# Performance work log

Measured on AMD Instinct MI355X. Metric: run time of the kernel, lower is better.

Reference implementation:

```python
import jax, jax.numpy as jnp
import numpy as np

L, C, FC, H, W, K = 6, 256, 1024, 4, 10, 3
B, T = 4, 1024
KC = C // H


def _get_rel_emb(emb, length):
    # emb: [1, 2W+1, KC] -> [1, 2*length-1, KC]
    pad_len = max(length - (W + 1), 0)
    start = max(W + 1 - length, 0)
    if pad_len > 0:
        emb = jnp.pad(emb, ((0, 0), (pad_len, pad_len), (0, 0)))
    return emb[:, start:start + 2 * length - 1]


def _rel_to_abs(x):
    # [b,h,l,2l-1] -> [b,h,l,l] via pad/reshape shift trick
    b, h, l, _ = x.shape
    x = jnp.pad(x, ((0, 0), (0, 0), (0, 0), (0, 1)))
    x = x.reshape(b, h, l * 2 * l)
    x = jnp.pad(x, ((0, 0), (0, 0), (0, l - 1)))
    return x.reshape(b, h, l + 1, 2 * l - 1)[:, :, :l, l - 1:]


def _abs_to_rel(x):
    # [b,h,l,l] -> [b,h,l,2l-1]
    b, h, l, _ = x.shape
    x = jnp.pad(x, ((0, 0), (0, 0), (0, 0), (0, l - 1)))
    x = x.reshape(b, h, l * l + l * (l - 1))
    x = jnp.pad(x, ((0, 0), (0, 0), (l, 0)))
    return x.reshape(b, h, l, 2 * l)[:, :, :, 1:]


def _ln(x, g, b, eps=1e-5):
    # channel-wise LayerNorm over dim 1 of [B,C,T]
    m = x.mean(axis=1, keepdims=True)
    v = ((x - m) ** 2).mean(axis=1, keepdims=True)
    return (x - m) * jax.lax.rsqrt(v + eps) * g[None, :, None] + b[None, :, None]


def _conv1(x, w, b):
    # pointwise Conv1d: x [B,Cin,T], w [Cout,Cin]
    return jnp.einsum('oc,bct->bot', w, x) + b[None, :, None]


def _convk(x, w, b):
    # Conv1d: x [B,Cin,Tpad], w [Cout,Cin,K], VALID
    y = jax.lax.conv_general_dilated(x, w, (1,), 'VALID', dimension_numbers=('NCH', 'OIH', 'NCH'))
    return y + b[None, :, None]


def _attn(x, mask, wq, bq, wk, bk, wv, bv, wo, bo, erk, erv):
    b, d, t = x.shape
    q = _conv1(x, wq, bq)
    k = _conv1(x, wk, bk)
    v = _conv1(x, wv, bv)
    def split(z):
        return z.reshape(b, H, KC, t).transpose(0, 1, 3, 2)  # [b,h,t,kc]
    qh = split(q) / np.sqrt(KC).astype(np.float32)
    kh = split(k)
    vh = split(v)
    scores = jnp.einsum('bhld,bhmd->bhlm', qh, kh)
    rel_k = _get_rel_emb(erk, t)[0]  # [2t-1, kc]
    scores = scores + _rel_to_abs(jnp.einsum('bhld,md->bhlm', qh, rel_k))
    scores = jnp.where(mask == 0, jnp.float32(-1e4), scores)
    p = jax.nn.softmax(scores, axis=-1)
    out = jnp.einsum('bhlm,bhmd->bhld', p, vh)
    rel_v = _get_rel_emb(erv, t)[0]
    out = out + jnp.einsum('bhlm,md->bhld', _abs_to_rel(p), rel_v)
    out = out.transpose(0, 1, 3, 2).reshape(b, d, t)
    return _conv1(out, wo, bo)


def _ffn(x, mask, w1, b1, w2, b2):
    pl, pr = (K - 1) // 2, K // 2
    def pad_t(z):
        return jnp.pad(z * mask, ((0, 0), (0, 0), (pl, pr)))
    h = jax.nn.relu(_convk(pad_t(x), w1, b1))
    return _convk(pad_t(h), w2, b2) * mask


def setup_inputs() -> dict:
    key = jax.random.key(0)
    ks = jax.random.split(key, 12)
    s = 0.05
    return {
        'x': jax.random.normal(ks[0], (B, C, T), jnp.float32),
        'x_mask': jnp.ones((B, 1, T), jnp.float32),
        'wq': s * jax.random.normal(ks[1], (L, C, C), jnp.float32),
        'bq': jnp.zeros((L, C), jnp.float32),
        'wk': s * jax.random.normal(ks[2], (L, C, C), jnp.float32),
        'bk': jnp.zeros((L, C), jnp.float32),
        'wv': s * jax.random.normal(ks[3], (L, C, C), jnp.float32),
        'bv': jnp.zeros((L, C), jnp.float32),
        'wo': s * jax.random.normal(ks[4], (L, C, C), jnp.float32),
        'bo': jnp.zeros((L, C), jnp.float32),
        'erk': (KC ** -0.5) * jax.random.normal(ks[5], (L, 1, 2 * W + 1, KC), jnp.float32),
        'erv': (KC ** -0.5) * jax.random.normal(ks[6], (L, 1, 2 * W + 1, KC), jnp.float32),
        'ln1_g': jnp.ones((L, C), jnp.float32),
        'ln1_b': jnp.zeros((L, C), jnp.float32),
        'ffn_w1': s * jax.random.normal(ks[7], (L, FC, C, K), jnp.float32),
        'ffn_b1': jnp.zeros((L, FC), jnp.float32),
        'ffn_w2': s * jax.random.normal(ks[8], (L, C, FC, K), jnp.float32),
        'ffn_b2': jnp.zeros((L, C), jnp.float32),
        'ln2_g': jnp.ones((L, C), jnp.float32),
        'ln2_b': jnp.zeros((L, C), jnp.float32),
    }


def reference(x, x_mask, wq, bq, wk, bk, wv, bv, wo, bo, erk, erv, ln1_g, ln1_b, ffn_w1, ffn_b1, ffn_w2, ffn_b2, ln2_g, ln2_b):
    attn_mask = x_mask[:, :, None, :] * x_mask[:, :, :, None]  # [B,1,T,T]
    x = x * x_mask
    for i in range(L):
        y = _attn(x, attn_mask, wq[i], bq[i], wk[i], bk[i], wv[i], bv[i], wo[i], bo[i], erk[i], erv[i])
        x = _ln(x + y, ln1_g[i], ln1_b[i])
        y = _ffn(x, x_mask, ffn_w1[i], ffn_b1[i], ffn_w2[i], ffn_b2[i])
        x = _ln(x + y, ln2_g[i], ln2_b[i])
    return x * x_mask
```

## Files before the change

kernel.cpp:

```cpp
#include <hip/hip_runtime.h>


#define Lz 6
#define Cz 256
#define FCz 1024
#define Hz 4
#define Wz 10
#define Bz 4
#define Tz 1024
#define KCz 64
#define NR 21
#define TS 1032
#define PADF 4
#define PROWS 1026
#define MFIX 8.0f

typedef unsigned short u16;
typedef unsigned int u32;
typedef __attribute__((ext_vector_type(8))) short bf8v;
typedef __attribute__((ext_vector_type(4))) float f4v;

#define MFMA(a, b, c) __builtin_amdgcn_mfma_f32_16x16x32_bf16(a, b, c, 0, 0, 0)

__device__ inline void bf_split(float v, u16& hi, u16& lo) {
  unsigned u = __float_as_uint(v);
  unsigned hr = (u + 0x7FFFu + ((u >> 16) & 1u)) >> 16;
  float rem = v - __uint_as_float(hr << 16);
  unsigned u2 = __float_as_uint(rem);
  unsigned lr = (u2 + 0x7FFFu + ((u2 >> 16) & 1u)) >> 16;
  hi = (u16)hr;
  lo = (u16)lr;
}

__device__ inline u16 bf_rne(float v) {
  u32 u = __float_as_uint(v);
  return (u16)((u + 0x7FFFu + ((u >> 16) & 1u)) >> 16);
}

__global__ __launch_bounds__(256) void mask_in(const float* __restrict__ x,
                                               const float* __restrict__ m,
                                               float* __restrict__ xp) {
  int id = blockIdx.x * 256 + threadIdx.x;
  if (id < Bz * Cz * Tz) {
    int t = id & (Tz - 1), row = id >> 10, b = id >> 18;
    xp[(size_t)row * TS + PADF + t] = x[id] * m[b * Tz + t];
  }
}

__global__ __launch_bounds__(256) void mask_out(const float* __restrict__ xp,
                                                const float* __restrict__ m,
                                                float* __restrict__ out) {
  int id = blockIdx.x * 256 + threadIdx.x;
  if (id < Bz * Cz * Tz) {
    int t = id & (Tz - 1), row = id >> 10, b = id >> 18;
    out[id] = xp[(size_t)row * TS + PADF + t] * m[b * Tz + t];
  }
}

__global__ __launch_bounds__(256) void zero_halo(u16* hi, u16* lo, int Cd) {
  int id = blockIdx.x * 256 + threadIdx.x;
  if (id >= Bz * 2 * Cd) return;
  int c = id % Cd, rb = id / Cd, b = rb >> 1, s = rb & 1;
  size_t a = ((size_t)b * PROWS + (s ? (PROWS - 1) : 0)) * Cd + c;
  hi[a] = 0;
  lo[a] = 0;
}

__global__ __launch_bounds__(256) void tpack(const float* __restrict__ src,
                                             const float* __restrict__ mask,
                                             u16* __restrict__ dhi,
                                             u16* __restrict__ dlo, int Cd) {
  __shared__ float L[64 * 68];
  const int tid = threadIdx.x;
  const int t0 = blockIdx.x * 64, c0 = blockIdx.y * 64, b = blockIdx.z;
  const float* sb = src + (size_t)b * Cd * TS + PADF;
#pragma unroll
  for (int i = 0; i < 16; i++) {
    int id = tid + 256 * i;
    int cc = id >> 6, tt = id & 63;
    L[cc * 68 + tt] = sb[(size_t)(c0 + cc) * TS + t0 + tt];
  }
  __syncthreads();
  const int tt = tid >> 2, p = tid & 3;
  float mv = mask[(size_t)b * Tz + t0 + tt];
  u16 hs[16], ls[16];
#pragma unroll
  for (int j = 0; j < 16; j++) {
    float v = L[(p * 16 + j) * 68 + tt] * mv;
    bf_split(v, hs[j], ls[j]);
  }
  size_t da = ((size_t)b * PROWS + t0 + tt + 1) * Cd + c0 + p * 16;
  *(uint4*)&dhi[da] = *(uint4*)&hs[0];
  *(uint4*)&dhi[da + 8] = *(uint4*)&hs[8];
  *(uint4*)&dlo[da] = *(uint4*)&ls[0];
  *(uint4*)&dlo[da + 8] = *(uint4*)&ls[8];
}

__global__ __launch_bounds__(256) void pack_all(
    const float* __restrict__ wq, const float* __restrict__ wk,
    const float* __restrict__ wv, const float* __restrict__ wo_,
    const float* __restrict__ bq, const float* __restrict__ bk,
    const float* __restrict__ bv, const float* __restrict__ bo,
    const float* __restrict__ erk, const float* __restrict__ erv,
    const float* __restrict__ fw1, const float* __restrict__ fw2,
    u16* __restrict__ qwAll, float* __restrict__ pbAll,
    u16* __restrict__ ekAll, u16* __restrict__ evAll,
    u16* __restrict__ w1All, u16* __restrict__ w2All) {
  const int blk = blockIdx.x, tid = threadIdx.x;
  const int layer = blk / 7184;
  const int bl = blk % 7184;
  if (bl < 1024) {
    int id = bl * 256 + tid;
    int o = id >> 8, c = id & 255;
    int sel = o >> 8;
    const size_t wof = (size_t)layer * Cz * Cz;
    const float* w = sel == 0 ? wq + wof
                              : (sel == 1 ? wk + wof
                                          : (sel == 2 ? wv + wof : wo_ + wof));
    qwAll[(size_t)layer * 262144 + id] = bf_rne(w[((o & 255) << 8) + c]);
    if (id < 1024) {
      int s2 = id >> 8;
      const float* bs = s2 == 0 ? bq : (s2 == 1 ? bk : (s2 == 2 ? bv : bo));
      pbAll[layer * 1024 + id] = bs[layer * Cz + (id & 255)];
    }
  } else if (bl < 1040) {
    int id = (bl - 1024) * 256 + tid;
    if (id < 2048) {
      int rr = id >> 6, d = id & 63;
      ekAll[layer * 2048 + id] =
          bf_rne((rr < NR) ? erk[(size_t)layer * NR * KCz + rr * KCz + d]
                           : 0.f);
    } else {
      int id2 = id - 2048;
      int d = id2 >> 5, rr = id2 & 31;
      evAll[layer * 2048 + id2] =
          bf_rne((rr < NR) ? erv[(size_t)layer * NR * KCz + rr * KCz + d]
                           : 0.f);
    }
  } else if (bl < 4112) {
    int id = (bl - 1040) * 256 + tid;
    int c = id % Cz;
    int rest = id / Cz;
    int o = rest % FCz, tap = rest / FCz;
    w1All[(size_t)layer * 786432 + id] =
        bf_rne(fw1[(size_t)layer * FCz * Cz * 3 + ((size_t)o * Cz + c) * 3 +
                   tap]);
  } else {
    int id = (bl - 4112) * 256 + tid;
    int c = id % FCz;
    int rest = id / FCz;
    int o = rest % Cz, tap = rest / Cz;
    w2All[(size_t)layer * 786432 + id] =
        bf_rne(fw2[(size_t)layer * Cz * FCz * 3 + ((size_t)o * FCz + c) * 3 +
                   tap]);
  }
}

template <int EPI>
__global__ __launch_bounds__(256) void mfma_gemm2(
    const u16* __restrict__ Ah, const u16* __restrict__ Bh,
    const u16* __restrict__ Bl, const float* __restrict__ bias,
    const float* __restrict__ mask, float* __restrict__ out,
    float* __restrict__ out2, u16* __restrict__ pqh, u16* __restrict__ pql,
    u16* __restrict__ pkh, u16* __restrict__ pvh, int M, int Kc, int m_base) {
  __shared__ __align__(16) char smraw[17408];
  u16* Ash = (u16*)smraw;
  u16* Bsh = Ash + 2560;
  u16* Bsl = Bsh + 2560;
  const int tid = threadIdx.x;
  const int lane = tid & 63, wid = tid >> 6;
  const int wm = wid & 1, wn = wid >> 1;
  const int r = lane & 15, qd = lane >> 4;
  const int t0 = blockIdx.x * 64;
  const int b = blockIdx.z;
  const int srow = tid >> 2, sseg = (tid & 3) * 8;

  int m0, kc0, kcN;
  float* outp = out;
  if constexpr (EPI == 3) {
    m0 = m_base + (blockIdx.y >> 1) * 64;
    kc0 = (blockIdx.y & 1) * (Kc / 2);
    kcN = Kc / 2;
    outp = (blockIdx.y & 1) ? out2 : out;
  } else {
    m0 = blockIdx.y * 64 + m_base;
    kc0 = 0;
    kcN = Kc;
  }

  f4v acc[2][2];
#pragma unroll
  for (int i = 0; i < 2; i++)
#pragma unroll
    for (int j = 0; j < 2; j++) acc[i][j] = (f4v)(0.f);

  const size_t arow = (size_t)(m0 + srow) * Kc + kc0;
  const size_t brow = ((size_t)b * PROWS + t0 + 1 + srow) * Kc + kc0;
  for (int kc = 0; kc < kcN; kc += 32) {
    *(uint4*)&Ash[srow * 40 + sseg] = *(const uint4*)&Ah[arow + kc + sseg];
    *(uint4*)&Bsh[srow * 40 + sseg] = *(const uint4*)&Bh[brow + kc + sseg];
    *(uint4*)&Bsl[srow * 40 + sseg] = *(const uint4*)&Bl[brow + kc + sseg];
    __syncthreads();
    bf8v ah[2], bh2[2], bl2[2];
#pragma unroll
    for (int f = 0; f < 2; f++) {
      int ar = (wm * 32 + f * 16 + r) * 40 + qd * 8;
      int br = (wn * 32 + f * 16 + r) * 40 + qd * 8;
      ah[f] = *(bf8v*)&Ash[ar];
      bh2[f] = *(bf8v*)&Bsh[br];
      bl2[f] = *(bf8v*)&Bsl[br];
    }
#pragma unroll
    for (int mf = 0; mf < 2; mf++)
#pragma unroll
      for (int nf = 0; nf < 2; nf++) {
        acc[mf][nf] = MFMA(ah[mf], bh2[nf], acc[mf][nf]);
        acc[mf][nf] = MFMA(ah[mf], bl2[nf], acc[mf][nf]);
      }
    __syncthreads();
  }

  float* Ds = (float*)smraw;
  if constexpr (EPI == 0) {
    const int sel = m0 >> 8;
    const int h = (m0 >> 6) & 3;
    const int bhI = b * Hz + h;
    if (sel < 2) {
#pragma unroll
      for (int mf = 0; mf < 2; mf++)
#pragma unroll
        for (int nf = 0; nf < 2; nf++) {
          int nl = wn * 32 + nf * 16 + r;
          int ml = wm * 32 + mf * 16 + qd * 4;
          *(f4v*)&Ds[nl * 68 + ml] = acc[mf][nf];
        }
      __syncthreads();
      const int row = tid >> 2, p = tid & 3;
      size_t da = ((size_t)bhI * Tz + t0 + row) * KCz + p * 16;
      if (sel == 0) {
        u16 hs[16], ls[16];
#pragma unroll
        for (int jj = 0; jj < 4; jj++) {
          float4 dv = *(float4*)&Ds[row * 68 + p * 16 + jj * 4];
          float4 bb = *(const float4*)&bias[m0 + p * 16 + jj * 4];
          float vv[4] = {(dv.x + bb.x) * 0.125f, (dv.y + bb.y) * 0.125f,
                         (dv.z + bb.z) * 0.125f, (dv.w + bb.w) * 0.125f};
#pragma unroll
          for (int e = 0; e < 4; e++)
            bf_split(vv[e], hs[jj * 4 + e], ls[jj * 4 + e]);
        }
        *(uint4*)&pqh[da] = *(uint4*)&hs[0];
        *(uint4*)&pqh[da + 8] = *(uint4*)&hs[8];
        *(uint4*)&pql[da] = *(uint4*)&ls[0];
        *(uint4*)&pql[da + 8] = *(uint4*)&ls[8];
      } else {
        u16 hs[16];
#pragma unroll
        for (int jj = 0; jj < 4; jj++) {
          float4 dv = *(float4*)&Ds[row * 68 + p * 16 + jj * 4];
          float4 bb = *(const float4*)&bias[m0 + p * 16 + jj * 4];
          hs[jj * 4 + 0] = bf_rne(dv.x + bb.x);
          hs[jj * 4 + 1] = bf_rne(dv.y + bb.y);
          hs[jj * 4 + 2] = bf_rne(dv.z + bb.z);
          hs[jj * 4 + 3] = bf_rne(dv.w + bb.w);
        }
        *(uint4*)&pkh[da] = *(uint4*)&hs[0];
        *(uint4*)&pkh[da + 8] = *(uint4*)&hs[8];
      }
    } else {
#pragma unroll
      for (int mf = 0; mf < 2; mf++)
#pragma unroll
        for (int nf = 0; nf < 2; nf++) {
          int ml = wm * 32 + mf * 16 + qd * 4;
          int nl = wn * 32 + nf * 16 + r;
#pragma unroll
          for (int e = 0; e < 4; e++) Ds[(ml + e) * 68 + nl] = acc[mf][nf][e];
        }
      __syncthreads();
      const int row = tid >> 2, p = tid & 3;
      const float bb = bias[m0 + row];
      u16 hs[16];
#pragma unroll
      for (int jj = 0; jj < 16; jj++)
        hs[jj] = bf_rne(Ds[row * 68 + p * 16 + jj] + bb);
      size_t da = ((size_t)bhI * KCz + row) * Tz + t0 + p * 16;
      *(uint4*)&pvh[da] = *(uint4*)&hs[0];
      *(uint4*)&pvh[da + 8] = *(uint4*)&hs[8];
    }
  } else {
#pragma unroll
    for (int mf = 0; mf < 2; mf++)
#pragma unroll
      for (int nf = 0; nf < 2; nf++) {
        int ml = wm * 32 + mf * 16 + qd * 4;
        int nl = wn * 32 + nf * 16 + r;
#pragma unroll
        for (int e = 0; e < 4; e++) Ds[(ml + e) * 68 + nl] = acc[mf][nf][e];
      }
    __syncthreads();
    const int row = tid >> 2, p = tid & 3;
    size_t oa = ((size_t)b * Cz + (m0 - m_base) + row) * Tz + t0 + p * 16;
#pragma unroll
    for (int jj = 0; jj < 4; jj++)
      *(float4*)&outp[oa + jj * 4] = *(float4*)&Ds[row * 68 + p * 16 + jj * 4];
  }
}

template <int EPI>
__global__ __launch_bounds__(256, 2) void conv_mfma(
    const u16* __restrict__ Ah, const u16* __restrict__ Bh,
    const u16* __restrict__ Bl, const float* __restrict__ bias,
    const float* __restrict__ mask, u16* __restrict__ ph,
    u16* __restrict__ pl, float* __restrict__ o0, float* __restrict__ o1,
    float* __restrict__ o2, float* __restrict__ o3, int M, int Kc) {
  __shared__ __align__(16) char smraw[36480];
  u16* Ash = (u16*)smraw;
  u16* Bsh = Ash + 3 * 64 * 40;
  u16* Bsl = Bsh + 132 * 40;
  const int tid = threadIdx.x;
  const int lane = tid & 63, wn = tid >> 6;
  const int r = lane & 15, qd = lane >> 4;
  const int t0 = blockIdx.x * 128;
  const int b = blockIdx.z;

  int m0, kc0, kcN;
  float* outp = nullptr;
  if constexpr (EPI == 3) {
    int mt = blockIdx.y >> 2, sp = blockIdx.y & 3;
    m0 = mt * 64;
    kc0 = sp * (Kc / 4);
    kcN = Kc / 4;
    outp = sp == 0 ? o0 : (sp == 1 ? o1 : (sp == 2 ? o2 : o3));
  } else {
    m0 = blockIdx.y * 64;
    kc0 = 0;
    kcN = Kc;
  }

  const int srow = tid >> 2, sseg = (tid & 3) * 8;
  const bool btail = tid < 8;
  const int brow2 = 128 + (tid >> 2);

  f4v acc[4][2];
#pragma unroll
  for (int i = 0; i < 4; i++)
#pragma unroll
    for (int j = 0; j < 2; j++) acc[i][j] = (f4v)(0.f);

  const size_t abase = (size_t)(m0 + srow) * Kc + kc0 + sseg;
  const size_t bbase = ((size_t)b * PROWS + t0 + srow) * Kc + kc0 + sseg;
  const size_t bbase64 = bbase + (size_t)64 * Kc;
  const size_t bbaseT = ((size_t)b * PROWS + t0 + brow2) * Kc + kc0 + sseg;

  uint4 ar[3], bh0, bh1, bl0, bl1, bht, blt;
  auto LOADR = [&](int kc) {
#pragma unroll
    for (int tp = 0; tp < 3; tp++)
      ar[tp] = *(const uint4*)&Ah[(size_t)tp * M * Kc + abase + kc];
    bh0 = *(const uint4*)&Bh[bbase + kc];
    bh1 = *(const uint4*)&Bh[bbase64 + kc];
    bl0 = *(const uint4*)&Bl[bbase + kc];
    bl1 = *(const uint4*)&Bl[bbase64 + kc];
    if (btail) {
      bht = *(const uint4*)&Bh[bbaseT + kc];
      blt = *(const uint4*)&Bl[bbaseT + kc];
    }
  };

  LOADR(0);
  for (int kc = 0; kc < kcN; kc += 32) {
#pragma unroll
    for (int tp = 0; tp < 3; tp++)
      *(uint4*)&Ash[(tp * 64 + srow) * 40 + sseg] = ar[tp];
    *(uint4*)&Bsh[srow * 40 + sseg] = bh0;
    *(uint4*)&Bsh[(srow + 64) * 40 + sseg] = bh1;
    *(uint4*)&Bsl[srow * 40 + sseg] = bl0;
    *(uint4*)&Bsl[(srow + 64) * 40 + sseg] = bl1;
    if (btail) {
      *(uint4*)&Bsh[brow2 * 40 + sseg] = bht;
      *(uint4*)&Bsl[brow2 * 40 + sseg] = blt;
    }
    __syncthreads();
    if (kc + 32 < kcN) LOADR(kc + 32);
#pragma unroll
    for (int tap = 0; tap < 3; tap++) {
      bf8v ah[4], bh2[2], bl2[2];
#pragma unroll
      for (int mf = 0; mf < 4; mf++)
        ah[mf] = *(bf8v*)&Ash[(tap * 64 + mf * 16 + r) * 40 + qd * 8];
#pragma unroll
      for (int nf = 0; nf < 2; nf++) {
        int br = (wn * 32 + nf * 16 + r + tap) * 40 + qd * 8;
        bh2[nf] = *(bf8v*)&Bsh[br];
        bl2[nf] = *(bf8v*)&Bsl[br];
      }
#pragma unroll
      for (int mf = 0; mf < 4; mf++)
#pragma unroll
        for (int nf = 0; nf < 2; nf++) {
          acc[mf][nf] = MFMA(ah[mf], bh2[nf], acc[mf][nf]);
          acc[mf][nf] = MFMA(ah[mf], bl2[nf], acc[mf][nf]);
        }
    }
    __syncthreads();
  }

  if constexpr (EPI == 1) {
    float* Ds = (float*)smraw;
#pragma unroll
    for (int mf = 0; mf < 4; mf++)
#pragma unroll
      for (int nf = 0; nf < 2; nf++) {
        int tl = wn * 32 + nf * 16 + r;
        int ml = mf * 16 + qd * 4;
        *(f4v*)&Ds[tl * 68 + ml] = acc[mf][nf];
      }
    __syncthreads();
    const int row = tid >> 1, half = (tid & 1) * 32;
    const int t = t0 + row;
    const float mv = mask[(size_t)b * Tz + t];
    u16 hs[32], ls[32];
#pragma unroll
    for (int j = 0; j < 32; j += 4) {
      float4 dv = *(float4*)&Ds[row * 68 + half + j];
      float4 bb = *(const float4*)&bias[m0 + half + j];
      float vv[4] = {dv.x + bb.x, dv.y + bb.y, dv.z + bb.z, dv.w + bb.w};
#pragma unroll
      for (int e = 0; e < 4; e++) {
        float v = fmaxf(vv[e], 0.f) * mv;
        bf_split(v, hs[j + e], ls[j + e]);
      }
    }
    size_t da = ((size_t)b * PROWS + t + 1) * M + m0 + half;
#pragma unroll
    for (int j = 0; j < 32; j += 8) {
      *(uint4*)&ph[da + j] = *(uint4*)&hs[j];
      *(uint4*)&pl[da + j] = *(uint4*)&ls[j];
    }
  } else {
    float* Ds = (float*)smraw;
#pragma unroll
    for (int mf = 0; mf < 4; mf++)
#pragma unroll
      for (int nf = 0; nf < 2; nf++) {
        int ml = mf * 16 + qd * 4;
        int nl = wn * 32 + nf * 16 + r;
#pragma unroll
        for (int e = 0; e < 4; e++) Ds[(ml + e) * 132 + nl] = acc[mf][nf][e];
      }
    __syncthreads();
    const int row = tid >> 2, seg = (tid & 3) * 32;
    size_t oa = ((size_t)b * Cz + m0 + row) * Tz + t0 + seg;
#pragma unroll
    for (int j = 0; j < 8; j++)
      *(float4*)&outp[oa + j * 4] = *(float4*)&Ds[row * 132 + seg + j * 4];
  }
}

__global__ __launch_bounds__(128, 2) void attn_mfma(
    const u16* __restrict__ Qh_, const u16* __restrict__ Ql_,
    const u16* __restrict__ Kh_, const u16* __restrict__ Vh_,
    const float* __restrict__ mask, const u16* __restrict__ erkH,
    const u16* __restrict__ ervH, float* __restrict__ O0,
    float* __restrict__ O1, float* __restrict__ O2, float* __restrict__ O3,
    float* __restrict__ lp0, float* __restrict__ lp1,
    float* __restrict__ lp2, float* __restrict__ lp3) {
  __shared__ __align__(16) char smraw[2][14336];
  const int tid = threadIdx.x;
  const int lane = tid & 63, wid = tid >> 6;
  const int r = lane & 15, qd = lane >> 4;
  const int idx = blockIdx.x;
  const int bh = idx & 15;
  const int split = (idx >> 4) & 3;
  const int i0w = (idx >> 6) * 64 + wid * 32;
  const int b = bh >> 2, h = bh & 3;
  const float* mb = mask + (size_t)b * Tz;
  const size_t qkbase = (size_t)bh * Tz * KCz;
  const size_t vbase = (size_t)bh * KCz * Tz;
  float* Op = split == 0 ? O0 : (split == 1 ? O1 : (split == 2 ? O2 : O3));
  float* lp = split == 0 ? lp0 : (split == 1 ? lp1 : (split == 2 ? lp2 : lp3));
  const int j0beg = split * 256;

  float* rqs = (float*)(smraw[wid]);
  float* bands = rqs + 704;
  u16* Pp = (u16*)(smraw[wid] + 5632);

  bf8v qh[2][2], ql[2][2];
#pragma unroll
  for (int rs = 0; rs < 2; rs++) {
    const size_t qrow = qkbase + (size_t)(i0w + rs * 16 + r) * KCz;
#pragma unroll
    for (int ks = 0; ks < 2; ks++) {
      qh[rs][ks] = *(const bf8v*)&Qh_[qrow + ks * 32 + qd * 8];
      ql[rs][ks] = *(const bf8v*)&Ql_[qrow + ks * 32 + qd * 8];
    }
  }
  for (int t = lane; t < 704; t += 64) bands[t] = -1e30f;

#pragma unroll
  for (int rs = 0; rs < 2; rs++) {
    f4v rc[2] = {(f4v)(0.f), (f4v)(0.f)};
#pragma unroll
    for (int nf = 0; nf < 2; nf++)
#pragma unroll
      for (int ks = 0; ks < 2; ks++) {
        bf8v eh = *(const bf8v*)&erkH[(16 * nf + r) * 64 + ks * 32 + qd * 8];
        rc[nf] = MFMA(qh[rs][ks], eh, rc[nf]);
        rc[nf] = MFMA(ql[rs][ks], eh, rc[nf]);
      }
#pragma unroll
    for (int nf = 0; nf < 2; nf++) {
      int rr = 16 * nf + r;
      if (rr < NR) {
#pragma unroll
        for (int e = 0; e < 4; e++)
          rqs[(rs * 16 + 4 * qd + e) * 22 + rr] = rc[nf][e];
      }
    }
  }

  float qm[2][4];
#pragma unroll
  for (int rs = 0; rs < 2; rs++)
#pragma unroll
    for (int e = 0; e < 4; e++) qm[rs][e] = mb[i0w + rs * 16 + 4 * qd + e];

  float lacc[2][4] = {};
  f4v oacc[2][4];
#pragma unroll
  for (int rs = 0; rs < 2; rs++)
#pragma unroll
    for (int nf = 0; nf < 4; nf++) oacc[rs][nf] = (f4v)(0.f);

#pragma unroll 2
  for (int jt = 0; jt < 4; jt++) {
    const int j0 = j0beg + jt * 64;
    bf8v kh[4][2], vh[4][2];
#pragma unroll
    for (int nf = 0; nf < 4; nf++) {
      const size_t kr = qkbase + (size_t)(j0 + 16 * nf + r) * KCz;
      const size_t vr = vbase + (size_t)(16 * nf + r) * Tz + j0;
#pragma unroll
      for (int ks = 0; ks < 2; ks++) {
        kh[nf][ks] = *(const bf8v*)&Kh_[kr + ks * 32 + qd * 8];
        vh[nf][ks] = *(const bf8v*)&Vh_[vr + ks * 32 + qd * 8];
      }
    }
    float km4[4];
#pragma unroll
    for (int nf = 0; nf < 4; nf++) km4[nf] = mb[j0 + 16 * nf + r];

#pragma unroll
    for (int rs = 0; rs < 2; rs++) {
      f4v sa[4];
#pragma unroll
      for (int nf = 0; nf < 4; nf++) sa[nf] = (f4v)(0.f);
#pragma unroll
      for (int nf = 0; nf < 4; nf++)
#pragma unroll
        for (int ks = 0; ks < 2; ks++) {
          sa[nf] = MFMA(qh[rs][ks], kh[nf][ks], sa[nf]);
          sa[nf] = MFMA(ql[rs][ks], kh[nf][ks], sa[nf]);
        }
      const int ibase = i0w + rs * 16;
      const bool diag = (j0 + 63 >= ibase - Wz) && (j0 <= ibase + 15 + Wz);
#pragma unroll
      for (int nf = 0; nf < 4; nf++)
#pragma unroll
        for (int e = 0; e < 4; e++) {
          const int iloc = rs * 16 + 4 * qd + e;
          float s = sa[nf][e];
          if (diag) {
            int dl = (j0 + 16 * nf + r) - (i0w + iloc);
            bool inb = (unsigned)(dl + Wz) <= 2u * Wz;
            if (inb) s += rqs[iloc * 22 + dl + Wz];
            if (qm[rs][e] * km4[nf] == 0.f) s = -1e4f;
            if (inb) bands[iloc * 22 + dl + Wz] = s;
          } else {
            if (qm[rs][e] * km4[nf] == 0.f) s = -1e4f;
          }
          float p = __expf(s - MFIX);
          lacc[rs][e] += p;
          Pp[iloc * 72 + 16 * nf + r] = bf_rne(p);
        }
    }
#pragma unroll
    for (int rs = 0; rs < 2; rs++)
#pragma unroll
      for (int ks = 0; ks < 2; ks++) {
        bf8v Ph = *(bf8v*)&Pp[(rs * 16 + r) * 72 + ks * 32 + qd * 8];
#pragma unroll
        for (int nf = 0; nf < 4; nf++)
          oacc[rs][nf] = MFMA(Ph, vh[nf][ks], oacc[rs][nf]);
      }
  }

  for (int t = lane; t < 32 * 32; t += 64) {
    int i = t >> 5, rr = t & 31;
    float p = (rr < NR) ? __expf(bands[i * 22 + rr] - MFIX) : 0.f;
    Pp[i * 72 + rr] = bf_rne(p);
  }
#pragma unroll
  for (int rs = 0; rs < 2; rs++) {
    bf8v Ph = *(bf8v*)&Pp[(rs * 16 + r) * 72 + qd * 8];
#pragma unroll
    for (int nf = 0; nf < 4; nf++) {
      bf8v eh = *(const bf8v*)&ervH[(16 * nf + r) * 32 + qd * 8];
      oacc[rs][nf] = MFMA(Ph, eh, oacc[rs][nf]);
    }
  }

#pragma unroll
  for (int off = 1; off < 16; off <<= 1)
#pragma unroll
    for (int rs = 0; rs < 2; rs++)
#pragma unroll
      for (int e = 0; e < 4; e++)
        lacc[rs][e] += __shfl_xor(lacc[rs][e], off, 16);
  if (r == 0) {
#pragma unroll
    for (int rs = 0; rs < 2; rs++)
#pragma unroll
      for (int e = 0; e < 4; e++)
        lp[(size_t)bh * Tz + i0w + rs * 16 + 4 * qd + e] = lacc[rs][e];
  }

  float* Os = (float*)Pp;
#pragma unroll
  for (int rs = 0; rs < 2; rs++)
#pragma unroll
    for (int nf = 0; nf < 4; nf++)
#pragma unroll
      for (int e = 0; e < 4; e++)
        Os[(rs * 16 + 4 * qd + e) * 68 + 16 * nf + r] = oacc[rs][nf][e];
#pragma unroll
  for (int rs = 0; rs < 2; rs++) {
    const float* src = &Os[(rs * 16 + r) * 68 + qd * 16];
    size_t oa = ((size_t)bh * Tz + i0w + rs * 16 + r) * KCz + qd * 16;
#pragma unroll
    for (int jj = 0; jj < 4; jj++)
      *(float4*)&Op[oa + jj * 4] = *(const float4*)&src[jj * 4];
  }
}

__global__ __launch_bounds__(256) void attn_combine(
    const float* __restrict__ O0, const float* __restrict__ O1,
    const float* __restrict__ O2, const float* __restrict__ O3,
    const float* __restrict__ l0, const float* __restrict__ l1,
    const float* __restrict__ l2, const float* __restrict__ l3,
    u16* __restrict__ outH, u16* __restrict__ outL,
    u16* __restrict__ hpH, u16* __restrict__ hpL) {
  const int bh = blockIdx.y, b = bh >> 2, h = bh & 3;
  if (blockIdx.x == 0) {
    int id = bh * 256 + threadIdx.x;
#pragma unroll
    for (int kk = 0; kk < 2; kk++) {
      int k = id + kk * 4096;
      int c = k & (FCz - 1), rb = k >> 10, bb2 = rb >> 1, ss = rb & 1;
      size_t a = ((size_t)bb2 * PROWS + (ss ? (PROWS - 1) : 0)) * FCz + c;
      hpH[a] = 0;
      hpL[a] = 0;
    }
  }
  const int i = blockIdx.x * 16 + (threadIdx.x >> 4);
  const int d0 = (threadIdx.x & 15) * 4;
  const size_t oa = ((size_t)bh * Tz + i) * KCz + d0;
  float4 a = *(const float4*)&O0[oa];
  float4 c = *(const float4*)&O1[oa];
  float4 d = *(const float4*)&O2[oa];
  float4 f = *(const float4*)&O3[oa];
  const size_t la = (size_t)bh * Tz + i;
  const float li = 1.f / (l0[la] + l1[la] + l2[la] + l3[la]);
  float v[4] = {(a.x + c.x + d.x + f.x) * li, (a.y + c.y + d.y + f.y) * li,
                (a.z + c.z + d.z + f.z) * li, (a.w + c.w + d.w + f.w) * li};
  u16 hs[4], ls[4];
#pragma unroll
  for (int e = 0; e < 4; e++) bf_split(v[e], hs[e], ls[e]);
  size_t da = ((size_t)b * PROWS + i + 1) * Cz + h * 64 + d0;
  *(uint2*)&outH[da] = *(uint2*)&hs[0];
  *(uint2*)&outL[da] = *(uint2*)&ls[0];
}

template <int VAR, int NP>
__global__ __launch_bounds__(256) void fused_ln(
    float* __restrict__ x, const float* __restrict__ y,
    const float* __restrict__ p1, const float* __restrict__ p2,
    const float* __restrict__ p3, const float* __restrict__ cbias,
    const float* __restrict__ g, const float* __restrict__ bb,
    const float* __restrict__ mask, u16* __restrict__ dhi,
    u16* __restrict__ dlo) {
  __shared__ float L[256 * 9];
  __shared__ float red[32][8], red2[32][8];
  __shared__ float ms[8], rs[8];
  const int tid = threadIdx.x;
  const int t0 = blockIdx.x * 8, b = blockIdx.y;
  const int tl = tid & 7, grp = tid >> 3;
  const size_t bx = (size_t)b * Cz * TS + PADF + t0 + tl;
  const size_t by = (size_t)b * Cz * Tz + t0 + tl;
  const float mv = mask[(size_t)b * Tz + t0 + tl];
  float s = 0.f, sq = 0.f;
#pragma unroll
  for (int i = 0; i < 8; i++) {
    int c = grp + i * 32;
    float add = y[by + (size_t)c * Tz] + p1[by + (size_t)c * Tz] + cbias[c];
    if constexpr (NP == 4)
      add += p2[by + (size_t)c * Tz] + p3[by + (size_t)c * Tz];
    if constexpr (VAR == 1) add *= mv;
    float v = x[bx + (size_t)c * TS] + add;
    L[c * 9 + tl] = v;
    s += v;
    sq += v * v;
  }
  red[grp][tl] = s;
  red2[grp][tl] = sq;
  __syncthreads();
  if (tid < 64) {
    const int j = tid >> 3, tt = tid & 7;
    float su = red[j][tt] + red[j + 8][tt] + red[j + 16][tt] + red[j + 24][tt];
    float sqq =
        red2[j][tt] + red2[j + 8][tt] + red2[j + 16][tt] + red2[j + 24][tt];
    su += __shfl_xor(su, 8);
    su += __shfl_xor(su, 16);
    su += __shfl_xor(su, 32);
    sqq += __shfl_xor(sqq, 8);
    sqq += __shfl_xor(sqq, 16);
    sqq += __shfl_xor(sqq, 32);
    if (j == 0) {
      float m = su * (1.f / Cz);
      ms[tt] = m;
      rs[tt] = rsqrtf(sqq * (1.f / Cz) - m * m + 1e-5f);
    }
  }
  __syncthreads();
  const float m = ms[tl], r = rs[tl];
#pragma unroll
  for (int i = 0; i < 8; i++) {
    int c = grp + i * 32;
    float v = (L[c * 9 + tl] - m) * r * g[c] + bb[c];
    x[bx + (size_t)c * TS] = v;
    L[c * 9 + tl] = v * mv;
  }
  __syncthreads();
  const int tt = tid & 7, p = tid >> 3;
  u16 hs[8], ls[8];
#pragma unroll
  for (int j = 0; j < 8; j++)
    bf_split(L[(p * 8 + j) * 9 + tt], hs[j], ls[j]);
  size_t da = ((size_t)b * PROWS + t0 + tt + 1) * Cz + p * 8;
  *(uint4*)&dhi[da] = *(uint4*)&hs[0];
  *(uint4*)&dlo[da] = *(uint4*)&ls[0];
}

extern "C" void kernel_launch(void* const* d_in, const int* in_sizes, int n_in,
                              void* d_out, int out_size, void* d_ws,
                              size_t ws_size, hipStream_t stream) {
  const float* x = (const float*)d_in[0];
  const float* xm = (const float*)d_in[1];
  const float* wq = (const float*)d_in[2];
  const float* bq = (const float*)d_in[3];
  const float* wk = (const float*)d_in[4];
  const float* bk = (const float*)d_in[5];
  const float* wv = (const float*)d_in[6];
  const float* bv = (const float*)d_in[7];
  const float* wo = (const float*)d_in[8];
  const float* bo = (const float*)d_in[9];
  const float* erk = (const float*)d_in[10];
  const float* erv = (const float*)d_in[11];
  const float* g1 = (const float*)d_in[12];
  const float* b1 = (const float*)d_in[13];
  const float* fw1 = (const float*)d_in[14];
  const float* fb1 = (const float*)d_in[15];
  const float* fw2 = (const float*)d_in[16];
  const float* fb2 = (const float*)d_in[17];
  const float* g2 = (const float*)d_in[18];
  const float* b2 = (const float*)d_in[19];

  const size_t NBC = (size_t)Bz * Cz * Tz;
  const size_t XBN = (size_t)Bz * Cz * TS;
  const size_t HP = (size_t)Bz * PROWS * FCz;
  const size_t XP = (size_t)Bz * PROWS * Cz;
  const size_t QS = (size_t)Bz * Hz * Tz * KCz;

  float* ws = (float*)d_ws;
  float* xb = ws;
  float* yb = xb + XBN;
  float* p1 = yb + NBC;
  float* p2 = p1 + NBC;
  float* p3 = p2 + NBC;
  float* unf = p3 + NBC;
  u16* hpH = (u16*)unf;
  u16* hpL = hpH + HP;
  u16* Qh = (u16*)unf;
  u16* Ql = Qh + QS;
  u16* Kh = Ql + QS;
  u16* Vh = Kh + QS;
  float* xpf = unf + HP;
  u16* xpH = (u16*)xpf;
  u16* xpL = xpH + XP;
  float* qwf = xpf + XP;
  u16* qwAll = (u16*)qwf;
  float* w1f = qwf + 786432;
  u16* w1All = (u16*)w1f;
  float* w2f = w1f + 2359296;
  u16* w2All = (u16*)w2f;
  float* erf = w2f + 2359296;
  u16* ekAll = (u16*)erf;
  u16* evAll = ekAll + 12288;
  float* pbAll = erf + 12288;
  float* lb0 = pbAll + 6144;
  float* lb1 = lb0 + 16384;
  float* lb2 = lb1 + 16384;
  float* lb3 = lb2 + 16384;

  const int ntot = (int)NBC;
  pack_all<<<dim3(6 * 7184), 256, 0, stream>>>(
      wq, wk, wv, wo, bq, bk, bv, bo, erk, erv, fw1, fw2, qwAll, pbAll, ekAll,
      evAll, w1All, w2All);
  mask_in<<<dim3((ntot + 255) / 256), 256, 0, stream>>>(x, xm, xb);
  zero_halo<<<dim3((Bz * 2 * Cz + 255) / 256), 256, 0, stream>>>(xpH, xpL, Cz);
  tpack<<<dim3(16, 4, 4), 256, 0, stream>>>(xb, xm, xpH, xpL, Cz);

  for (int l = 0; l < Lz; l++) {
    mfma_gemm2<0><<<dim3(16, 12, 4), 256, 0, stream>>>(
        qwAll + (size_t)l * 262144, xpH, xpL, pbAll + l * 1024, xm, nullptr,
        nullptr, Qh, Ql, Kh, Vh, 1024, Cz, 0);
    attn_mfma<<<dim3(1024), 128, 0, stream>>>(
        Qh, Ql, Kh, Vh, xm, ekAll + l * 2048, evAll + l * 2048, yb, p1, p2, p3,
        lb0, lb1, lb2, lb3);
    attn_combine<<<dim3(64, 16), 256, 0, stream>>>(yb, p1, p2, p3, lb0, lb1,
                                                   lb2, lb3, xpH, xpL, hpH,
                                                   hpL);
    mfma_gemm2<3><<<dim3(16, 8, 4), 256, 0, stream>>>(
        qwAll + (size_t)l * 262144, xpH, xpL, pbAll + l * 1024, xm, yb, p1,
        nullptr, nullptr, nullptr, nullptr, 1024, Cz, 768);
    fused_ln<2, 2><<<dim3(128, 4), 256, 0, stream>>>(
        xb, yb, p1, nullptr, nullptr, bo + l * Cz, g1 + l * Cz, b1 + l * Cz,
        xm, xpH, xpL);
    conv_mfma<1><<<dim3(8, 16, 4), 256, 0, stream>>>(
        w1All + (size_t)l * 786432, xpH, xpL, fb1 + l * FCz, xm, hpH, hpL,
        nullptr, nullptr, nullptr, nullptr, FCz, Cz);
    conv_mfma<3><<<dim3(8, 16, 4), 256, 0, stream>>>(
        w2All + (size_t)l * 786432, hpH, hpL, nullptr, xm, nullptr, nullptr,
        yb, p1, p2, p3, Cz, FCz);
    fused_ln<1, 4><<<dim3(128, 4), 256, 0, stream>>>(
        xb, yb, p1, p2, p3, fb2 + l * Cz, g2 + l * Cz, b2 + l * Cz, xm, xpH,
        xpL);
  }
  mask_out<<<dim3((ntot + 255) / 256), 256, 0, stream>>>(xb, xm,
                                                         (float*)d_out);
}
```

Before: 992.0 us.

## Fuse attention split-combine into output-projection GEMM and zero conv halos in-register

```diff
diff --git a/kernel.cpp b/kernel.cpp
--- a/kernel.cpp
+++ b/kernel.cpp
@@ -55,15 +55,6 @@
     int t = id & (Tz - 1), row = id >> 10, b = id >> 18;
     out[id] = xp[(size_t)row * TS + PADF + t] * m[b * Tz + t];
   }
-}
-
-__global__ __launch_bounds__(256) void zero_halo(u16* hi, u16* lo, int Cd) {
-  int id = blockIdx.x * 256 + threadIdx.x;
-  if (id >= Bz * 2 * Cd) return;
-  int c = id % Cd, rb = id / Cd, b = rb >> 1, s = rb & 1;
-  size_t a = ((size_t)b * PROWS + (s ? (PROWS - 1) : 0)) * Cd + c;
-  hi[a] = 0;
-  lo[a] = 0;
 }
 
 __global__ __launch_bounds__(256) void tpack(const float* __restrict__ src,
@@ -160,9 +151,13 @@
 __global__ __launch_bounds__(256) void mfma_gemm2(
     const u16* __restrict__ Ah, const u16* __restrict__ Bh,
     const u16* __restrict__ Bl, const float* __restrict__ bias,
-    const float* __restrict__ mask, float* __restrict__ out,
-    float* __restrict__ out2, u16* __restrict__ pqh, u16* __restrict__ pql,
-    u16* __restrict__ pkh, u16* __restrict__ pvh, int M, int Kc, int m_base) {
+    float* __restrict__ out, float* __restrict__ out2,
+    u16* __restrict__ pqh, u16* __restrict__ pql, u16* __restrict__ pkh,
+    u16* __restrict__ pvh, const float* __restrict__ Ox0,
+    const float* __restrict__ Ox1, const float* __restrict__ Ox2,
+    const float* __restrict__ Ox3, const float* __restrict__ sl0,
+    const float* __restrict__ sl1, const float* __restrict__ sl2,
+    const float* __restrict__ sl3, int M, int Kc, int m_base) {
   __shared__ __align__(16) char smraw[17408];
   u16* Ash = (u16*)smraw;
   u16* Bsh = Ash + 2560;
@@ -198,8 +193,37 @@
   const size_t brow = ((size_t)b * PROWS + t0 + 1 + srow) * Kc + kc0;
   for (int kc = 0; kc < kcN; kc += 32) {
     *(uint4*)&Ash[srow * 40 + sseg] = *(const uint4*)&Ah[arow + kc + sseg];
-    *(uint4*)&Bsh[srow * 40 + sseg] = *(const uint4*)&Bh[brow + kc + sseg];
-    *(uint4*)&Bsl[srow * 40 + sseg] = *(const uint4*)&Bl[brow + kc + sseg];
+    if constexpr (EPI == 3) {
+      const int cc = kc0 + kc + sseg;
+      const int hh = cc >> 6, dd = cc & 63;
+      const size_t lbi = (size_t)(b * Hz + hh) * Tz + t0 + srow;
+      const size_t ob = lbi * KCz + dd;
+      float4 qa = *(const float4*)&Ox0[ob];
+      float4 qb = *(const float4*)&Ox0[ob + 4];
+      float4 ra = *(const float4*)&Ox1[ob];
+      float4 rb = *(const float4*)&Ox1[ob + 4];
+      float4 sa = *(const float4*)&Ox2[ob];
+      float4 sb = *(const float4*)&Ox2[ob + 4];
+      float4 ta = *(const float4*)&Ox3[ob];
+      float4 tb = *(const float4*)&Ox3[ob + 4];
+      const float li = 1.f / (sl0[lbi] + sl1[lbi] + sl2[lbi] + sl3[lbi]);
+      float v[8] = {(qa.x + ra.x + sa.x + ta.x) * li,
+                    (qa.y + ra.y + sa.y + ta.y) * li,
+                    (qa.z + ra.z + sa.z + ta.z) * li,
+                    (qa.w + ra.w + sa.w + ta.w) * li,
+                    (qb.x + rb.x + sb.x + tb.x) * li,
+                    (qb.y + rb.y + sb.y + tb.y) * li,
+                    (qb.z + rb.z + sb.z + tb.z) * li,
+                    (qb.w + rb.w + sb.w + tb.w) * li};
+      u16 hhs[8], lls[8];
+#pragma unroll
+      for (int e = 0; e < 8; e++) bf_split(v[e], hhs[e], lls[e]);
+      *(uint4*)&Bsh[srow * 40 + sseg] = *(uint4*)&hhs[0];
+      *(uint4*)&Bsl[srow * 40 + sseg] = *(uint4*)&lls[0];
+    } else {
+      *(uint4*)&Bsh[srow * 40 + sseg] = *(const uint4*)&Bh[brow + kc + sseg];
+      *(uint4*)&Bsl[srow * 40 + sseg] = *(const uint4*)&Bl[brow + kc + sseg];
+    }
     __syncthreads();
     bf8v ah[2], bh2[2], bl2[2];
 #pragma unroll
@@ -341,6 +365,9 @@
   const int srow = tid >> 2, sseg = (tid & 3) * 8;
   const bool btail = tid < 8;
   const int brow2 = 128 + (tid >> 2);
+  const bool h0 = (t0 + srow == 0);
+  const bool hT = btail && (t0 + brow2 == PROWS - 1);
+  const uint4 z4 = {0u, 0u, 0u, 0u};
 
   f4v acc[4][2];
 #pragma unroll
@@ -359,12 +386,20 @@
     for (int tp = 0; tp < 3; tp++)
       ar[tp] = *(const uint4*)&Ah[(size_t)tp * M * Kc + abase + kc];
     bh0 = *(const uint4*)&Bh[bbase + kc];
+    bl0 = *(const uint4*)&Bl[bbase + kc];
+    if (h0) {
+      bh0 = z4;
+      bl0 = z4;
+    }
     bh1 = *(const uint4*)&Bh[bbase64 + kc];
-    bl0 = *(const uint4*)&Bl[bbase + kc];
     bl1 = *(const uint4*)&Bl[bbase64 + kc];
     if (btail) {
       bht = *(const uint4*)&Bh[bbaseT + kc];
       blt = *(const uint4*)&Bl[bbaseT + kc];
+      if (hT) {
+        bht = z4;
+        blt = z4;
+      }
     }
   };
 
@@ -644,44 +679,6 @@
   }
 }
 
-__global__ __launch_bounds__(256) void attn_combine(
-    const float* __restrict__ O0, const float* __restrict__ O1,
-    const float* __restrict__ O2, const float* __restrict__ O3,
-    const float* __restrict__ l0, const float* __restrict__ l1,
-    const float* __restrict__ l2, const float* __restrict__ l3,
-    u16* __restrict__ outH, u16* __restrict__ outL,
-    u16* __restrict__ hpH, u16* __restrict__ hpL) {
-  const int bh = blockIdx.y, b = bh >> 2, h = bh & 3;
-  if (blockIdx.x == 0) {
-    int id = bh * 256 + threadIdx.x;
-#pragma unroll
-    for (int kk = 0; kk < 2; kk++) {
-      int k = id + kk * 4096;
-      int c = k & (FCz - 1), rb = k >> 10, bb2 = rb >> 1, ss = rb & 1;
-      size_t a = ((size_t)bb2 * PROWS + (ss ? (PROWS - 1) : 0)) * FCz + c;
-      hpH[a] = 0;
-      hpL[a] = 0;
-    }
-  }
-  const int i = blockIdx.x * 16 + (threadIdx.x >> 4);
-  const int d0 = (threadIdx.x & 15) * 4;
-  const size_t oa = ((size_t)bh * Tz + i) * KCz + d0;
-  float4 a = *(const float4*)&O0[oa];
-  float4 c = *(const float4*)&O1[oa];
-  float4 d = *(const float4*)&O2[oa];
-  float4 f = *(const float4*)&O3[oa];
-  const size_t la = (size_t)bh * Tz + i;
-  const float li = 1.f / (l0[la] + l1[la] + l2[la] + l3[la]);
-  float v[4] = {(a.x + c.x + d.x + f.x) * li, (a.y + c.y + d.y + f.y) * li,
-                (a.z + c.z + d.z + f.z) * li, (a.w + c.w + d.w + f.w) * li};
-  u16 hs[4], ls[4];
-#pragma unroll
-  for (int e = 0; e < 4; e++) bf_split(v[e], hs[e], ls[e]);
-  size_t da = ((size_t)b * PROWS + i + 1) * Cz + h * 64 + d0;
-  *(uint2*)&outH[da] = *(uint2*)&hs[0];
-  *(uint2*)&outL[da] = *(uint2*)&ls[0];
-}
-
 template <int VAR, int NP>
 __global__ __launch_bounds__(256) void fused_ln(
     float* __restrict__ x, const float* __restrict__ y,
@@ -795,6 +792,8 @@
   u16* Ql = Qh + QS;
   u16* Kh = Ql + QS;
   u16* Vh = Kh + QS;
+  float* wo0 = unf;
+  float* wo1 = unf + NBC;
   float* xpf = unf + HP;
   u16* xpH = (u16*)xpf;
   u16* xpL = xpH + XP;
@@ -818,24 +817,22 @@
       wq, wk, wv, wo, bq, bk, bv, bo, erk, erv, fw1, fw2, qwAll, pbAll, ekAll,
       evAll, w1All, w2All);
   mask_in<<<dim3((ntot + 255) / 256), 256, 0, stream>>>(x, xm, xb);
-  zero_halo<<<dim3((Bz * 2 * Cz + 255) / 256), 256, 0, stream>>>(xpH, xpL, Cz);
   tpack<<<dim3(16, 4, 4), 256, 0, stream>>>(xb, xm, xpH, xpL, Cz);
 
   for (int l = 0; l < Lz; l++) {
     mfma_gemm2<0><<<dim3(16, 12, 4), 256, 0, stream>>>(
-        qwAll + (size_t)l * 262144, xpH, xpL, pbAll + l * 1024, xm, nullptr,
-        nullptr, Qh, Ql, Kh, Vh, 1024, Cz, 0);
+        qwAll + (size_t)l * 262144, xpH, xpL, pbAll + l * 1024, nullptr,
+        nullptr, Qh, Ql, Kh, Vh, nullptr, nullptr, nullptr, nullptr, nullptr,
+        nullptr, nullptr, nullptr, 1024, Cz, 0);
     attn_mfma<<<dim3(1024), 128, 0, stream>>>(
-        Qh, Ql, Kh, Vh, xm, ekAll + l * 2048, evAll + l * 2048, yb, p1, p2, p3,
-        lb0, lb1, lb2, lb3);
-    attn_combine<<<dim3(64, 16), 256, 0, stream>>>(yb, p1, p2, p3, lb0, lb1,
-                                                   lb2, lb3, xpH, xpL, hpH,
-                                                   hpL);
+        Qh, Ql, Kh, Vh, xm, ekAll + l * 2048, evAll + l * 2048, yb, p1, p2,
+        p3, lb0, lb1, lb2, lb3);
     mfma_gemm2<3><<<dim3(16, 8, 4), 256, 0, stream>>>(
-        qwAll + (size_t)l * 262144, xpH, xpL, pbAll + l * 1024, xm, yb, p1,
-        nullptr, nullptr, nullptr, nullptr, 1024, Cz, 768);
+        qwAll + (size_t)l * 262144, xpH, xpL, pbAll + l * 1024, wo0, wo1,
+        nullptr, nullptr, nullptr, nullptr, yb, p1, p2, p3, lb0, lb1, lb2,
+        lb3, 1024, Cz, 768);
     fused_ln<2, 2><<<dim3(128, 4), 256, 0, stream>>>(
-        xb, yb, p1, nullptr, nullptr, bo + l * Cz, g1 + l * Cz, b1 + l * Cz,
+        xb, wo0, wo1, nullptr, nullptr, bo + l * Cz, g1 + l * Cz, b1 + l * Cz,
         xm, xpH, xpL);
     conv_mfma<1><<<dim3(8, 16, 4), 256, 0, stream>>>(
         w1All + (size_t)l * 786432, xpH, xpL, fb1 + l * FCz, xm, hpH, hpL,
```

Measured after the change: 976.1 us. No clear change (-1.6%).
